# Kernel optimization log

Measured on AMD Instinct MI355X. Metric: run time of the kernel, lower is better.

The kernel has to match this reference:

```python
import jax, jax.numpy as jnp
import numpy as np

B, C, D, H, W = 2, 128, 16, 16, 16
NH = 4
HD = C // NH
GROUPS = 32
EPS = 1e-5


def group_norm(x, w, b):
    # x: [B, C, D, H, W]; normalize over (C/GROUPS, D, H, W) per group
    Bb, Cc = x.shape[0], x.shape[1]
    xr = x.reshape(Bb, GROUPS, -1)
    mu = xr.mean(axis=-1, keepdims=True)
    var = xr.var(axis=-1, keepdims=True)
    xn = ((xr - mu) * jax.lax.rsqrt(var + EPS)).reshape(x.shape)
    return xn * w.reshape(1, Cc, 1, 1, 1) + b.reshape(1, Cc, 1, 1, 1)


def setup_inputs() -> dict:
    key = jax.random.key(0)
    k0, k1, k2 = jax.random.split(key, 3)
    x = jax.random.normal(k0, (B, C, D, H, W), dtype=jnp.float32)
    gn_w = jnp.ones((C,), dtype=jnp.float32)
    gn_b = jnp.zeros((C,), dtype=jnp.float32)
    # 1x1x1 Conv3d weights as [out_ch, in_ch] matrices
    qkv_w = jax.random.normal(k1, (3 * C, C), dtype=jnp.float32) / np.sqrt(C).astype(np.float32)
    qkv_b = jnp.zeros((3 * C,), dtype=jnp.float32)
    out_w = jax.random.normal(k2, (C, C), dtype=jnp.float32) / np.sqrt(C).astype(np.float32)
    out_b = jnp.zeros((C,), dtype=jnp.float32)
    return {"x": x, "gn_w": gn_w, "gn_b": gn_b, "qkv_w": qkv_w, "qkv_b": qkv_b,
            "out_w": out_w, "out_b": out_b}


def reference(x, gn_w, gn_b, qkv_w, qkv_b, out_w, out_b):
    Bb, Cc, Dd, Hh, Ww = x.shape
    N = Dd * Hh * Ww
    scale = HD ** (-0.5)

    xn = group_norm(x, gn_w, gn_b)
    xf = xn.reshape(Bb, Cc, N)                              # [B, C, N]
    qkv = jnp.einsum('oc,bcn->bon', qkv_w, xf) + qkv_b[None, :, None]
    qkv = qkv.reshape(Bb, 3, NH, HD, N)
    q, k, v = qkv[:, 0], qkv[:, 1], qkv[:, 2]               # each [B, h, hd, N]

    attn = jnp.einsum('bhdn,bhdm->bhnm', q, k) * scale      # [B, h, N, N]
    attn = jax.nn.softmax(attn, axis=-1)
    o = jnp.einsum('bhnm,bhdm->bhdn', attn, v)              # [B, h, hd, N]
    o = o.reshape(Bb, Cc, N)

    y = jnp.einsum('oc,bcn->bon', out_w, o) + out_b[None, :, None]
    return y.reshape(Bb, Cc, Dd, Hh, Ww) + x
```

## Files before the change

### kernel.cpp

```cpp
#include <hip/hip_runtime.h>
#include <hip/hip_bf16.h>

#define B_ 2
#define C_ 128
#define N_ 4096
#define NH_ 4
#define HD_ 32
#define GROUPS_ 32
#define EPS_ 1e-5f
#define SCALE2_ 0.25503486f
#define NCH_ 4
#define CHKV_ 1024
#define NT_ (CHKV_ / 64)

typedef __attribute__((ext_vector_type(2))) float f32x2;
typedef __attribute__((ext_vector_type(4))) float f32x4;
typedef __attribute__((ext_vector_type(8))) short s16x8;
typedef __attribute__((ext_vector_type(2))) unsigned int u32x2;
typedef __attribute__((ext_vector_type(4))) unsigned int u32x4;
typedef unsigned short u16;
typedef unsigned int u32;

static __device__ __forceinline__ u32 cvtpk_bf16(float lo, float hi) {
  u32 r;
  asm("v_cvt_pk_bf16_f32 %0, %1, %2" : "=v"(r) : "v"(lo), "v"(hi));
  return r;
}
static __device__ __forceinline__ float fexp2(float x) {
  float r;
  asm("v_exp_f32 %0, %1" : "=v"(r) : "v"(x));
  return r;
}
static __device__ __forceinline__ float bflo(u32 w) { return __uint_as_float(w << 16); }
static __device__ __forceinline__ float bfhi(u32 w) { return __uint_as_float(w & 0xffff0000u); }

__global__ __launch_bounds__(256) void k_groupnorm(
    const float* __restrict__ x, const float* __restrict__ gw,
    const float* __restrict__ gb, u16* __restrict__ xn) {
  const int blk = blockIdx.x;
  const int tid = threadIdx.x;
  const size_t base = (size_t)blk * (4 * N_);
  const f32x4* x4 = (const f32x4*)(x + base);
  float s = 0.f, ss = 0.f;
  for (int i = tid; i < 4096; i += 256) {
    f32x4 v = x4[i];
    s  += v.x + v.y + v.z + v.w;
    ss += v.x*v.x + v.y*v.y + v.z*v.z + v.w*v.w;
  }
  for (int off = 32; off; off >>= 1) {
    s  += __shfl_down(s, off);
    ss += __shfl_down(ss, off);
  }
  __shared__ float red[2][4];
  __shared__ float mv[2];
  const int wid = tid >> 6;
  if ((tid & 63) == 0) { red[0][wid] = s; red[1][wid] = ss; }
  __syncthreads();
  if (tid == 0) {
    float S = red[0][0]+red[0][1]+red[0][2]+red[0][3];
    float Q = red[1][0]+red[1][1]+red[1][2]+red[1][3];
    float mu  = S * (1.f/16384.f);
    float var = Q * (1.f/16384.f) - mu*mu;
    mv[0] = mu; mv[1] = rsqrtf(var + EPS_);
  }
  __syncthreads();
  const float mu = mv[0], rs = mv[1];
  const int gi = blk & (GROUPS_ - 1);
  u32x2* xn2 = (u32x2*)(xn + base);
  for (int i = tid; i < 4096; i += 256) {
    const int c = gi*4 + (i >> 10);
    const float a  = gw[c] * rs;
    const float b2 = gb[c] - mu * a;
    f32x4 v = x4[i];
    f32x4 r = v * a + b2;
    u32x2 p = { cvtpk_bf16(r.x, r.y), cvtpk_bf16(r.z, r.w) };
    xn2[i] = p;
  }
}

__global__ __launch_bounds__(256) void k_gemm_qkv(
    const u16* __restrict__ xn, const float* __restrict__ w,
    const float* __restrict__ bias, u16* __restrict__ qkvb,
    u16* __restrict__ Kt) {
  const int tid = threadIdx.x;
  const int n0 = blockIdx.x * 512 + tid * 2;
  const int o0 = blockIdx.y * 8;
  const int b  = blockIdx.z;
  const u16* xb = xn + (size_t)b * C_ * N_;
  const float* wp = w + (size_t)o0 * C_;
  float ax[8] = {0,0,0,0,0,0,0,0};
  float ay[8] = {0,0,0,0,0,0,0,0};
  #pragma unroll 4
  for (int c = 0; c < C_; ++c) {
    const u32 wv = *(const u32*)(xb + (size_t)c * N_ + n0);
    const float x0 = bflo(wv), x1 = bfhi(wv);
    #pragma unroll
    for (int i = 0; i < 8; ++i) {
      const float wi = wp[(size_t)i * C_ + c];
      ax[i] += x0 * wi;
      ay[i] += x1 * wi;
    }
  }
  #pragma unroll
  for (int i = 0; i < 8; ++i) {
    const float bi = bias[o0 + i];
    ax[i] += bi; ay[i] += bi;
  }
  if (o0 < 128) {
    u16* op = qkvb + ((size_t)b * 384 + o0) * N_ + n0;
    #pragma unroll
    for (int i = 0; i < 8; ++i)
      *(u32*)(op + (size_t)i * N_) = cvtpk_bf16(ax[i] * SCALE2_, ay[i] * SCALE2_);
  } else if (o0 < 256) {
    const int h  = (o0 - 128) >> 5;
    const int d8 = (o0 - 128) & 31;
    u16* kb = Kt + (size_t)(b * NH_ + h) * N_ * HD_ + d8;
    u32x4 pk0 = { cvtpk_bf16(ax[0], ax[1]), cvtpk_bf16(ax[2], ax[3]),
                  cvtpk_bf16(ax[4], ax[5]), cvtpk_bf16(ax[6], ax[7]) };
    u32x4 pk1 = { cvtpk_bf16(ay[0], ay[1]), cvtpk_bf16(ay[2], ay[3]),
                  cvtpk_bf16(ay[4], ay[5]), cvtpk_bf16(ay[6], ay[7]) };
    *(u32x4*)(kb + (size_t)n0 * HD_)       = pk0;
    *(u32x4*)(kb + (size_t)(n0 + 1) * HD_) = pk1;
  } else {
    u16* op = qkvb + ((size_t)b * 384 + o0) * N_ + n0;
    #pragma unroll
    for (int i = 0; i < 8; ++i)
      *(u32*)(op + (size_t)i * N_) = cvtpk_bf16(ax[i], ay[i]);
  }
}

#define QTILE_STEP(qf, oa0, oa1, oL)                                           \
  {                                                                            \
    f32x4 s0 = __builtin_amdgcn_mfma_f32_16x16x32_bf16(ck0, qf, z, 0, 0, 0);   \
    f32x4 s1 = __builtin_amdgcn_mfma_f32_16x16x32_bf16(ck1, qf, z, 0, 0, 0);   \
    f32x4 s2 = __builtin_amdgcn_mfma_f32_16x16x32_bf16(ck2, qf, z, 0, 0, 0);   \
    f32x4 s3 = __builtin_amdgcn_mfma_f32_16x16x32_bf16(ck3, qf, z, 0, 0, 0);   \
    float p0 = fexp2(s0.x), p1 = fexp2(s0.y), p2 = fexp2(s0.z), p3 = fexp2(s0.w); \
    float p4 = fexp2(s1.x), p5 = fexp2(s1.y), p6 = fexp2(s1.z), p7 = fexp2(s1.w); \
    float p8 = fexp2(s2.x), p9 = fexp2(s2.y), pa_ = fexp2(s2.z), pb_ = fexp2(s2.w); \
    float pc_ = fexp2(s3.x), pd_ = fexp2(s3.y), pe_ = fexp2(s3.z), pf_ = fexp2(s3.w); \
    union { u32x4 u; s16x8 s; } pkA, pkB;                                      \
    pkA.u.x = cvtpk_bf16(p0, p1);   pkA.u.y = cvtpk_bf16(p2, p3);              \
    pkA.u.z = cvtpk_bf16(p4, p5);   pkA.u.w = cvtpk_bf16(p6, p7);              \
    pkB.u.x = cvtpk_bf16(p8, p9);   pkB.u.y = cvtpk_bf16(pa_, pb_);            \
    pkB.u.z = cvtpk_bf16(pc_, pd_); pkB.u.w = cvtpk_bf16(pe_, pf_);            \
    oa0 = __builtin_amdgcn_mfma_f32_16x16x32_bf16(pkA.s, cv0, oa0, 0, 0, 0);   \
    oa1 = __builtin_amdgcn_mfma_f32_16x16x32_bf16(pkA.s, cv1, oa1, 0, 0, 0);   \
    oL  = __builtin_amdgcn_mfma_f32_16x16x32_bf16(pkA.s, onesB, oL, 0, 0, 0);  \
    oa0 = __builtin_amdgcn_mfma_f32_16x16x32_bf16(pkB.s, cv2, oa0, 0, 0, 0);   \
    oa1 = __builtin_amdgcn_mfma_f32_16x16x32_bf16(pkB.s, cv3, oa1, 0, 0, 0);   \
    oL  = __builtin_amdgcn_mfma_f32_16x16x32_bf16(pkB.s, onesB, oL, 0, 0, 0);  \
  }

__global__ __launch_bounds__(256) void k_attn(
    const u16* __restrict__ qkvb, const u16* __restrict__ Kt,
    float* __restrict__ Opart, float* __restrict__ Lpart) {
  __shared__ u16 Kl[64 * 32];
  __shared__ u16 Vl[32 * 72];
  const int b = blockIdx.z, h = blockIdx.y;
  const int qt = blockIdx.x & 15, ch = blockIdx.x >> 4;
  const int tid = threadIdx.x;
  const int wid = tid >> 6, lane = tid & 63;
  const int g = lane >> 4, lq = lane & 15;
  const int q0 = qt * 256 + wid * 16;
  const int kv0 = ch * CHKV_;

  const u16* qb = qkvb + ((size_t)b * 384 + h * HD_) * N_;
  s16x8 qfA, qfB, qfC, qfD;
  #pragma unroll
  for (int j = 0; j < 8; ++j) {
    const u16* qr = qb + (size_t)(8*g + j) * N_ + q0 + lq;
    qfA[j] = (short)qr[0];
    qfB[j] = (short)qr[64];
    qfC[j] = (short)qr[128];
    qfD[j] = (short)qr[192];
  }

  const u16* ktb = Kt + (size_t)(b * NH_ + h) * N_ * HD_;
  const u16* vbb = qkvb + ((size_t)b * 384 + 256 + h * HD_) * N_;
  const int pi = ((lq >> 2) << 3) + (lq & 3);

  const u16* kst = ktb + (size_t)kv0 * HD_ + tid * 8;
  const int vrow = tid >> 3;
  const int vcol = (tid & 7) * 8;
  const u16* vst = vbb + (size_t)vrow * N_ + kv0 + vcol;
  u16* kdst = Kl + ((tid * 8) ^ (((tid >> 5) & 3) * 8));
  u16* vdst = Vl + vrow * 72 + vcol;

  const int xsw  = (pi >> 3) & 3;
  const int slot = 8 * (g ^ xsw);
  const int ka0 = (pi)      * 32 + slot;
  const int ka1 = (pi + 4)  * 32 + slot;
  const int ka2 = (pi + 32) * 32 + slot;
  const int ka3 = (pi + 36) * 32 + slot;
  const int va0 = lq * 72 + 8*g;
  const int va1 = (lq + 16) * 72 + 8*g;

  const short one_bf = (short)0x3F80;
  const s16x8 onesB = {one_bf, one_bf, one_bf, one_bf,
                       one_bf, one_bf, one_bf, one_bf};

  f32x4 oa0A = {0.f,0.f,0.f,0.f}, oa1A = oa0A, oLA = oa0A;
  f32x4 oa0B = oa0A, oa1B = oa0A, oLB = oa0A;
  f32x4 oa0C = oa0A, oa1C = oa0A, oLC = oa0A;
  f32x4 oa0D = oa0A, oa1D = oa0A, oLD = oa0A;

  {
    s16x8 kr = *(const s16x8*)(kst);
    s16x8 vr = *(const s16x8*)(vst);
    *(s16x8*)(kdst) = kr;
    *(s16x8*)(vdst) = vr;
  }
  __syncthreads();

  for (int tt = 0; tt < NT_; ++tt) {
    const int tn = (tt + 1 < NT_) ? (tt + 1) : (NT_ - 1);
    s16x8 kr = *(const s16x8*)(kst + (size_t)tn * 64 * HD_);
    s16x8 vr = *(const s16x8*)(vst + (size_t)tn * 64);

    const s16x8 ck0 = *(const s16x8*)(Kl + ka0);
    const s16x8 ck1 = *(const s16x8*)(Kl + ka1);
    const s16x8 ck2 = *(const s16x8*)(Kl + ka2);
    const s16x8 ck3 = *(const s16x8*)(Kl + ka3);
    const s16x8 cv0 = *(const s16x8*)(Vl + va0);
    const s16x8 cv1 = *(const s16x8*)(Vl + va1);
    const s16x8 cv2 = *(const s16x8*)(Vl + va0 + 32);
    const s16x8 cv3 = *(const s16x8*)(Vl + va1 + 32);

    const f32x4 z = {0.f,0.f,0.f,0.f};
    QTILE_STEP(qfA, oa0A, oa1A, oLA)
    QTILE_STEP(qfB, oa0B, oa1B, oLB)
    QTILE_STEP(qfC, oa0C, oa1C, oLC)
    QTILE_STEP(qfD, oa0D, oa1D, oLD)

    __syncthreads();
    *(s16x8*)(kdst) = kr;
    *(s16x8*)(vdst) = vr;
    __syncthreads();
  }

  const int bh = b * NH_ + h;
  float* opb = Opart + ((size_t)ch * (B_ * NH_) + bh) * ((size_t)N_ * HD_);
  #pragma unroll
  for (int r = 0; r < 4; ++r) {
    const int qrow = q0 + g*4 + r;
    opb[(size_t)qrow * HD_ + lq]              = oa0A[r];
    opb[(size_t)qrow * HD_ + lq + 16]         = oa1A[r];
    opb[(size_t)(qrow + 64) * HD_ + lq]       = oa0B[r];
    opb[(size_t)(qrow + 64) * HD_ + lq + 16]  = oa1B[r];
    opb[(size_t)(qrow + 128) * HD_ + lq]      = oa0C[r];
    opb[(size_t)(qrow + 128) * HD_ + lq + 16] = oa1C[r];
    opb[(size_t)(qrow + 192) * HD_ + lq]      = oa0D[r];
    opb[(size_t)(qrow + 192) * HD_ + lq + 16] = oa1D[r];
  }
  if (lq == 0) {
    float* lp = Lpart + ((size_t)ch * (B_ * NH_) + bh) * N_ + q0 + g*4;
    lp[0]   = oLA[0]; lp[1]   = oLA[1]; lp[2]   = oLA[2]; lp[3]   = oLA[3];
    lp[64]  = oLB[0]; lp[65]  = oLB[1]; lp[66]  = oLB[2]; lp[67]  = oLB[3];
    lp[128] = oLC[0]; lp[129] = oLC[1]; lp[130] = oLC[2]; lp[131] = oLC[3];
    lp[192] = oLD[0]; lp[193] = oLD[1]; lp[194] = oLD[2]; lp[195] = oLD[3];
  }
}

__global__ __launch_bounds__(256) void k_out(
    const float* __restrict__ Opart, const float* __restrict__ Lpart,
    const float* __restrict__ w, const float* __restrict__ bias,
    const float* __restrict__ x, float* __restrict__ y) {
  __shared__ u16 Ot[128][136];
  __shared__ float linv[NH_][128];
  const int t = threadIdx.x;
  const int n0 = blockIdx.x * 128;
  const int o0 = blockIdx.y * 16;
  const int b  = blockIdx.z;

  if (t < 128) {
    #pragma unroll
    for (int h = 0; h < NH_; ++h) {
      float s = 0.f;
      #pragma unroll
      for (int c = 0; c < NCH_; ++c)
        s += Lpart[((size_t)c * (B_ * NH_) + b * NH_ + h) * N_ + n0 + t];
      linv[h][t] = 1.0f / s;
    }
  }
  __syncthreads();

  {
    const int dd = (t & 7) * 4;
    const int nb = t >> 3;
    #pragma unroll
    for (int h = 0; h < NH_; ++h) {
      const float* ob = Opart + (size_t)(b * NH_ + h) * ((size_t)N_ * HD_)
                      + (size_t)n0 * HD_ + dd;
      #pragma unroll
      for (int p = 0; p < 4; ++p) {
        const int nn = p * 32 + nb;
        f32x4 a = {0.f,0.f,0.f,0.f};
        #pragma unroll
        for (int c = 0; c < NCH_; ++c)
          a += *(const f32x4*)(ob + (size_t)c * ((size_t)B_ * NH_ * N_ * HD_)
                                  + (size_t)nn * HD_);
        const float iv = linv[h][nn];
        a *= iv;
        Ot[32*h + dd + 0][nn] = (u16)cvtpk_bf16(a.x, a.x);
        Ot[32*h + dd + 1][nn] = (u16)cvtpk_bf16(a.y, a.y);
        Ot[32*h + dd + 2][nn] = (u16)cvtpk_bf16(a.z, a.z);
        Ot[32*h + dd + 3][nn] = (u16)cvtpk_bf16(a.w, a.w);
      }
    }
  }
  __syncthreads();

  const int n4  = (t & 31) * 4;
  const int orow = o0 + (t >> 5) * 2;
  const float* w0p = w + (size_t)orow * C_;
  const float* w1p = w0p + C_;
  f32x4 acc0 = {0.f,0.f,0.f,0.f}, acc1 = acc0;
  #pragma unroll 4
  for (int c = 0; c < C_; ++c) {
    const u32x2 ov = *(const u32x2*)(&Ot[c][n4]);
    const f32x4 xv = { bflo(ov.x), bfhi(ov.x), bflo(ov.y), bfhi(ov.y) };
    acc0 += xv * w0p[c];
    acc1 += xv * w1p[c];
  }
  const size_t yo = ((size_t)b * C_ + orow) * N_ + n0 + n4;
  const f32x4 xr0 = *(const f32x4*)(x + yo);
  const f32x4 xr1 = *(const f32x4*)(x + yo + N_);
  *(f32x4*)(y + yo)      = acc0 + bias[orow]     + xr0;
  *(f32x4*)(y + yo + N_) = acc1 + bias[orow + 1] + xr1;
}

extern "C" void kernel_launch(void* const* d_in, const int* in_sizes, int n_in,
                              void* d_out, int out_size, void* d_ws, size_t ws_size,
                              hipStream_t stream) {
  const float* x     = (const float*)d_in[0];
  const float* gn_w  = (const float*)d_in[1];
  const float* gn_b  = (const float*)d_in[2];
  const float* qkv_w = (const float*)d_in[3];
  const float* qkv_b = (const float*)d_in[4];
  const float* out_w = (const float*)d_in[5];
  const float* out_b = (const float*)d_in[6];
  float* y = (float*)d_out;

  float* ws  = (float*)d_ws;
  u16*   xn   = (u16*)ws;
  u16*   qkvb = (u16*)(ws + 524288);
  u16*   Kt   = (u16*)(ws + 2097152);
  float* Opart = ws + 2621440;
  float* Lpart = ws + 6815744;

  k_groupnorm<<<dim3(B_ * GROUPS_), 256, 0, stream>>>(x, gn_w, gn_b, xn);
  k_gemm_qkv <<<dim3(8, 48, B_),    256, 0, stream>>>(xn, qkv_w, qkv_b, qkvb, Kt);
  k_attn     <<<dim3(16 * NCH_, NH_, B_), 256, 0, stream>>>(qkvb, Kt, Opart, Lpart);
  k_out      <<<dim3(32, 8, B_),    256, 0, stream>>>(Opart, Lpart, out_w, out_b, x, y);
}
```

Measured before the change: 75.42 us.

## Store attention partials as bf16, widen groupnorm blocks, double k_out rows per thread

Attention partial outputs are stored as bf16 instead of fp32, halving the write and read traffic between the attention and output-projection kernels. Groupnorm now runs 1024 threads per block with unrolled loops, which gives more parallelism across its only 64 blocks. Each thread in the output projection now computes four output rows, halving the grid and the redundant Opart reduction work per block. The bf16 partials lose precision before the cross-chunk sum, and the smaller k_out grid lowers occupancy.

```diff
diff --git a/kernel.cpp b/kernel.cpp
--- a/kernel.cpp
+++ b/kernel.cpp
@@ -33,8 +33,9 @@
 }
 static __device__ __forceinline__ float bflo(u32 w) { return __uint_as_float(w << 16); }
 static __device__ __forceinline__ float bfhi(u32 w) { return __uint_as_float(w & 0xffff0000u); }
-
-__global__ __launch_bounds__(256) void k_groupnorm(
+static __device__ __forceinline__ u16 f2bf16(float f) { return (u16)cvtpk_bf16(f, f); }
+
+__global__ __launch_bounds__(1024) void k_groupnorm(
     const float* __restrict__ x, const float* __restrict__ gw,
     const float* __restrict__ gb, u16* __restrict__ xn) {
   const int blk = blockIdx.x;
@@ -42,7 +43,8 @@
   const size_t base = (size_t)blk * (4 * N_);
   const f32x4* x4 = (const f32x4*)(x + base);
   float s = 0.f, ss = 0.f;
-  for (int i = tid; i < 4096; i += 256) {
+  #pragma unroll
+  for (int i = tid; i < 4096; i += 1024) {
     f32x4 v = x4[i];
     s  += v.x + v.y + v.z + v.w;
     ss += v.x*v.x + v.y*v.y + v.z*v.z + v.w*v.w;
@@ -51,14 +53,15 @@
     s  += __shfl_down(s, off);
     ss += __shfl_down(ss, off);
   }
-  __shared__ float red[2][4];
+  __shared__ float red[2][16];
   __shared__ float mv[2];
   const int wid = tid >> 6;
   if ((tid & 63) == 0) { red[0][wid] = s; red[1][wid] = ss; }
   __syncthreads();
   if (tid == 0) {
-    float S = red[0][0]+red[0][1]+red[0][2]+red[0][3];
-    float Q = red[1][0]+red[1][1]+red[1][2]+red[1][3];
+    float S = 0.f, Q = 0.f;
+    #pragma unroll
+    for (int i = 0; i < 16; ++i) { S += red[0][i]; Q += red[1][i]; }
     float mu  = S * (1.f/16384.f);
     float var = Q * (1.f/16384.f) - mu*mu;
     mv[0] = mu; mv[1] = rsqrtf(var + EPS_);
@@ -67,7 +70,8 @@
   const float mu = mv[0], rs = mv[1];
   const int gi = blk & (GROUPS_ - 1);
   u32x2* xn2 = (u32x2*)(xn + base);
-  for (int i = tid; i < 4096; i += 256) {
+  #pragma unroll
+  for (int i = tid; i < 4096; i += 1024) {
     const int c = gi*4 + (i >> 10);
     const float a  = gw[c] * rs;
     const float b2 = gb[c] - mu * a;
@@ -154,7 +158,7 @@
 
 __global__ __launch_bounds__(256) void k_attn(
     const u16* __restrict__ qkvb, const u16* __restrict__ Kt,
-    float* __restrict__ Opart, float* __restrict__ Lpart) {
+    u16* __restrict__ Opart, float* __restrict__ Lpart) {
   __shared__ u16 Kl[64 * 32];
   __shared__ u16 Vl[32 * 72];
   const int b = blockIdx.z, h = blockIdx.y;
@@ -240,18 +244,18 @@
   }
 
   const int bh = b * NH_ + h;
-  float* opb = Opart + ((size_t)ch * (B_ * NH_) + bh) * ((size_t)N_ * HD_);
+  u16* opb = Opart + ((size_t)ch * (B_ * NH_) + bh) * ((size_t)N_ * HD_);
   #pragma unroll
   for (int r = 0; r < 4; ++r) {
     const int qrow = q0 + g*4 + r;
-    opb[(size_t)qrow * HD_ + lq]              = oa0A[r];
-    opb[(size_t)qrow * HD_ + lq + 16]         = oa1A[r];
-    opb[(size_t)(qrow + 64) * HD_ + lq]       = oa0B[r];
-    opb[(size_t)(qrow + 64) * HD_ + lq + 16]  = oa1B[r];
-    opb[(size_t)(qrow + 128) * HD_ + lq]      = oa0C[r];
-    opb[(size_t)(qrow + 128) * HD_ + lq + 16] = oa1C[r];
-    opb[(size_t)(qrow + 192) * HD_ + lq]      = oa0D[r];
-    opb[(size_t)(qrow + 192) * HD_ + lq + 16] = oa1D[r];
+    opb[(size_t)qrow * HD_ + lq]              = f2bf16(oa0A[r]);
+    opb[(size_t)qrow * HD_ + lq + 16]         = f2bf16(oa1A[r]);
+    opb[(size_t)(qrow + 64) * HD_ + lq]       = f2bf16(oa0B[r]);
+    opb[(size_t)(qrow + 64) * HD_ + lq + 16]  = f2bf16(oa1B[r]);
+    opb[(size_t)(qrow + 128) * HD_ + lq]      = f2bf16(oa0C[r]);
+    opb[(size_t)(qrow + 128) * HD_ + lq + 16] = f2bf16(oa1C[r]);
+    opb[(size_t)(qrow + 192) * HD_ + lq]      = f2bf16(oa0D[r]);
+    opb[(size_t)(qrow + 192) * HD_ + lq + 16] = f2bf16(oa1D[r]);
   }
   if (lq == 0) {
     float* lp = Lpart + ((size_t)ch * (B_ * NH_) + bh) * N_ + q0 + g*4;
@@ -263,14 +267,14 @@
 }
 
 __global__ __launch_bounds__(256) void k_out(
-    const float* __restrict__ Opart, const float* __restrict__ Lpart,
+    const u16* __restrict__ Opart, const float* __restrict__ Lpart,
     const float* __restrict__ w, const float* __restrict__ bias,
     const float* __restrict__ x, float* __restrict__ y) {
   __shared__ u16 Ot[128][136];
   __shared__ float linv[NH_][128];
   const int t = threadIdx.x;
   const int n0 = blockIdx.x * 128;
-  const int o0 = blockIdx.y * 16;
+  const int o0 = blockIdx.y * 32;
   const int b  = blockIdx.z;
 
   if (t < 128) {
@@ -290,44 +294,52 @@
     const int nb = t >> 3;
     #pragma unroll
     for (int h = 0; h < NH_; ++h) {
-      const float* ob = Opart + (size_t)(b * NH_ + h) * ((size_t)N_ * HD_)
-                      + (size_t)n0 * HD_ + dd;
+      const u16* ob = Opart + (size_t)(b * NH_ + h) * ((size_t)N_ * HD_)
+                    + (size_t)n0 * HD_ + dd;
       #pragma unroll
       for (int p = 0; p < 4; ++p) {
         const int nn = p * 32 + nb;
         f32x4 a = {0.f,0.f,0.f,0.f};
         #pragma unroll
-        for (int c = 0; c < NCH_; ++c)
-          a += *(const f32x4*)(ob + (size_t)c * ((size_t)B_ * NH_ * N_ * HD_)
-                                  + (size_t)nn * HD_);
+        for (int c = 0; c < NCH_; ++c) {
+          const u32x2 ov = *(const u32x2*)(ob
+              + (size_t)c * ((size_t)B_ * NH_ * N_ * HD_) + (size_t)nn * HD_);
+          a.x += bflo(ov.x); a.y += bfhi(ov.x);
+          a.z += bflo(ov.y); a.w += bfhi(ov.y);
+        }
         const float iv = linv[h][nn];
         a *= iv;
-        Ot[32*h + dd + 0][nn] = (u16)cvtpk_bf16(a.x, a.x);
-        Ot[32*h + dd + 1][nn] = (u16)cvtpk_bf16(a.y, a.y);
-        Ot[32*h + dd + 2][nn] = (u16)cvtpk_bf16(a.z, a.z);
-        Ot[32*h + dd + 3][nn] = (u16)cvtpk_bf16(a.w, a.w);
+        Ot[32*h + dd + 0][nn] = f2bf16(a.x);
+        Ot[32*h + dd + 1][nn] = f2bf16(a.y);
+        Ot[32*h + dd + 2][nn] = f2bf16(a.z);
+        Ot[32*h + dd + 3][nn] = f2bf16(a.w);
       }
     }
   }
   __syncthreads();
 
   const int n4  = (t & 31) * 4;
-  const int orow = o0 + (t >> 5) * 2;
-  const float* w0p = w + (size_t)orow * C_;
-  const float* w1p = w0p + C_;
-  f32x4 acc0 = {0.f,0.f,0.f,0.f}, acc1 = acc0;
+  const int orow = o0 + (t >> 5) * 4;
+  const float* wp = w + (size_t)orow * C_;
+  f32x4 acc0 = {0.f,0.f,0.f,0.f}, acc1 = acc0, acc2 = acc0, acc3 = acc0;
   #pragma unroll 4
   for (int c = 0; c < C_; ++c) {
     const u32x2 ov = *(const u32x2*)(&Ot[c][n4]);
     const f32x4 xv = { bflo(ov.x), bfhi(ov.x), bflo(ov.y), bfhi(ov.y) };
-    acc0 += xv * w0p[c];
-    acc1 += xv * w1p[c];
+    acc0 += xv * wp[c];
+    acc1 += xv * wp[C_ + c];
+    acc2 += xv * wp[2*C_ + c];
+    acc3 += xv * wp[3*C_ + c];
   }
   const size_t yo = ((size_t)b * C_ + orow) * N_ + n0 + n4;
   const f32x4 xr0 = *(const f32x4*)(x + yo);
   const f32x4 xr1 = *(const f32x4*)(x + yo + N_);
-  *(f32x4*)(y + yo)      = acc0 + bias[orow]     + xr0;
-  *(f32x4*)(y + yo + N_) = acc1 + bias[orow + 1] + xr1;
+  const f32x4 xr2 = *(const f32x4*)(x + yo + 2*N_);
+  const f32x4 xr3 = *(const f32x4*)(x + yo + 3*N_);
+  *(f32x4*)(y + yo)        = acc0 + bias[orow]     + xr0;
+  *(f32x4*)(y + yo + N_)   = acc1 + bias[orow + 1] + xr1;
+  *(f32x4*)(y + yo + 2*N_) = acc2 + bias[orow + 2] + xr2;
+  *(f32x4*)(y + yo + 3*N_) = acc3 + bias[orow + 3] + xr3;
 }
 
 extern "C" void kernel_launch(void* const* d_in, const int* in_sizes, int n_in,
@@ -346,11 +358,11 @@
   u16*   xn   = (u16*)ws;
   u16*   qkvb = (u16*)(ws + 524288);
   u16*   Kt   = (u16*)(ws + 2097152);
-  float* Opart = ws + 2621440;
-  float* Lpart = ws + 6815744;
-
-  k_groupnorm<<<dim3(B_ * GROUPS_), 256, 0, stream>>>(x, gn_w, gn_b, xn);
+  u16*   Opart = (u16*)(ws + 2621440);
+  float* Lpart = ws + 4718592;
+
+  k_groupnorm<<<dim3(B_ * GROUPS_), 1024, 0, stream>>>(x, gn_w, gn_b, xn);
   k_gemm_qkv <<<dim3(8, 48, B_),    256, 0, stream>>>(xn, qkv_w, qkv_b, qkvb, Kt);
   k_attn     <<<dim3(16 * NCH_, NH_, B_), 256, 0, stream>>>(qkvb, Kt, Opart, Lpart);
-  k_out      <<<dim3(32, 8, B_),    256, 0, stream>>>(Opart, Lpart, out_w, out_b, x, y);
-}
+  k_out      <<<dim3(32, 4, B_),    256, 0, stream>>>(Opart, Lpart, out_w, out_b, x, y);
+}
```

After: 68.43 us (median of 2 runs). 9.3% less time.
